# Kernel tuning notes

Measured on AMD Instinct MI355X. Metric: run time of the kernel, lower is better.

The kernel has to match this reference:

```python
import jax, jax.numpy as jnp
import numpy as np

VEC_DIM = 3          # Cl(3,0): 3 positive-signature basis vectors
BASIS_DIM = 1 << VEC_DIM  # 8 basis blades
BATCH, IN_F, OUT_F = 512, 512, 512


def cayley_table(n: int = VEC_DIM) -> np.ndarray:
    """Geometric-product tensor G[i, j, k] for Cl(n,0) with blades as bitmasks.
    e_a * e_b = sign(a,b) * e_{a XOR b}; Euclidean metric so e_i^2 = +1.
    Only 2^(2n) of the 2^(3n) entries are nonzero (highly sparse)."""
    dim = 1 << n
    G = np.zeros((dim, dim, dim), dtype=np.float32)
    for a in range(dim):
        for b in range(dim):
            # sign from counting transpositions to bring blade product to canonical order
            swaps, t = 0, a >> 1
            while t:
                swaps += bin(t & b).count("1")
                t >>= 1
            G[a, b, a ^ b] = -1.0 if (swaps & 1) else 1.0
    return G


def setup_inputs() -> dict:
    key = jax.random.key(0)
    kx, kw, kb = jax.random.split(key, 3)
    x = jax.random.normal(kx, (BATCH, IN_F, BASIS_DIM), dtype=jnp.float32)
    W = jax.random.normal(kw, (IN_F, OUT_F, BASIS_DIM), dtype=jnp.float32)
    b = jax.random.normal(kb, (OUT_F, BASIS_DIM), dtype=jnp.float32)
    G = jnp.asarray(cayley_table())  # exact Cl(3,0) geometric-product tensor
    return {"x": x, "W": W, "b": b, "G": G}


def reference(x, W, b, G):
    # out[b,o,k] = sum_{i,j,p} G[i,j,k] * x[b,p,i] * W[p,o,j]  (+ bias)
    out = jnp.einsum("ijk,bpi,poj->bok", G, x, W)
    return out + b
```

## Files before the change

kernel.cpp:

```cpp
#include <hip/hip_runtime.h>
#include <hip/hip_bf16.h>
#include <stdint.h>

typedef __attribute__((ext_vector_type(8))) short short8;
typedef __attribute__((ext_vector_type(4))) float floatx4;

__device__ __forceinline__ uint32_t pkbf(float a, float b) {
    unsigned short lo = __builtin_bit_cast(unsigned short, __float2bfloat16(a));
    unsigned short hi = __builtin_bit_cast(unsigned short, __float2bfloat16(b));
    return (uint32_t)lo | ((uint32_t)hi << 16);
}

__device__ __forceinline__ int gp_sign_neg(int a, int b) {
    int sw = 0, tt = a >> 1;
    while (tt) { sw += __popc(tt & b); tt >>= 1; }
    return sw & 1;
}

__global__ __launch_bounds__(256) void make_xT(const float* __restrict__ x,
                                               unsigned short* __restrict__ xT) {
    __shared__ unsigned short tile[8 * 512];
    const int b = blockIdx.x;
    const int t = threadIdx.x;
    const float4* xb = (const float4*)(x + (size_t)b * 4096);
    float4 f0 = xb[4 * t + 0], f1 = xb[4 * t + 1], f2 = xb[4 * t + 2], f3 = xb[4 * t + 3];
    float a0[8] = {f0.x, f0.y, f0.z, f0.w, f1.x, f1.y, f1.z, f1.w};
    float a1[8] = {f2.x, f2.y, f2.z, f2.w, f3.x, f3.y, f3.z, f3.w};
    uint32_t* tl = (uint32_t*)tile;
    #pragma unroll
    for (int i = 0; i < 8; ++i)
        tl[i * 256 + t] = pkbf(a0[i], a1[i]);
    __syncthreads();
    uint4* dst = (uint4*)(xT + (size_t)b * 4096);
    const uint4* src = (const uint4*)tile;
    dst[t] = src[t];
    dst[t + 256] = src[t + 256];
}

__global__ __launch_bounds__(256) void make_WT(const float* __restrict__ W,
                                               unsigned short* __restrict__ WT) {
    __shared__ unsigned short tile[8 * 64 * 24];
    const int t = threadIdx.x;
    const int o0 = blockIdx.x * 64, p0 = blockIdx.y * 16;
    const int o = t & 63, pq = t >> 6;
    float v[4][8];
    #pragma unroll
    for (int s = 0; s < 4; ++s) {
        const float4* src = (const float4*)(W + ((size_t)(p0 + pq * 4 + s) * 512 + o0 + o) * 8);
        float4 lo = src[0], hi = src[1];
        v[s][0] = lo.x; v[s][1] = lo.y; v[s][2] = lo.z; v[s][3] = lo.w;
        v[s][4] = hi.x; v[s][5] = hi.y; v[s][6] = hi.z; v[s][7] = hi.w;
    }
    #pragma unroll
    for (int j = 0; j < 8; ++j) {
        uint32_t* p = (uint32_t*)&tile[(j * 64 + o) * 24 + pq * 4];
        p[0] = pkbf(v[0][j], v[1][j]);
        p[1] = pkbf(v[2][j], v[3][j]);
    }
    __syncthreads();
    #pragma unroll
    for (int si = 0; si < 4; ++si) {
        int c = si * 256 + t;
        int j = c >> 7, oo = (c >> 1) & 63, h = c & 1;
        uint4 val = *(const uint4*)&tile[(j * 64 + oo) * 24 + h * 8];
        *(uint4*)&WT[((size_t)j * 512 + o0 + oo) * 512 + p0 + h * 8] = val;
    }
}

#define GLL(src, dstoff) \
    __builtin_amdgcn_global_load_lds((const __attribute__((address_space(1))) uint32_t*)(src), \
        (__attribute__((address_space(3))) uint32_t*)(smem + (dstoff)), 16, 0, 0)

__global__ __launch_bounds__(512, 2) void gp_gemm(
    const unsigned short* __restrict__ xT,
    const unsigned short* __restrict__ WT,
    const float* __restrict__ bias,
    float*       __restrict__ out)
{
    __shared__ __align__(16) unsigned char smem[81920];
    const int t = threadIdx.x;
    const int lane = t & 63;
    const int wave = t >> 6;
    const int wm = wave & 1;
    const int g  = wave >> 1;
    const int j0 = (g & 1) * 4;
    const int c0 = (g >> 1) * 2;
    const int l15 = lane & 15;
    const int q = lane >> 4;

    const int lin = blockIdx.y * 32 + blockIdx.x;
    const int cx = lin & 7, sx = lin >> 3;
    const int n_tile = (cx & 3) * 2 + (sx & 1);
    const int m_tile = (cx >> 2) * 16 + (sx >> 1);
    const int m0 = m_tile * 128;
    const int n0 = n_tile * 64;
    const int bg0 = m0 >> 3;

    const int sa_b = t >> 5, sa_i = (t >> 2) & 7, sa_cs = t & 3;
    const int sa_cl = sa_cs ^ ((sa_i & 3) ^ ((sa_i >> 2) & 1));
    const unsigned short* a_src = xT + ((size_t)(bg0 + sa_b) * 8 + sa_i) * 512 + sa_cl * 8;
    const unsigned short* b_srcs[4];
    #pragma unroll
    for (int si = 0; si < 4; ++si) {
        int s = si * 512 + t;
        int j = s >> 8, n = (s >> 2) & 63, cs = s & 3;
        int cl = cs ^ ((n >> 1) & 3);
        b_srcs[si] = WT + ((size_t)j * 512 + n0 + n) * 512 + cl * 8;
    }

    const int k_l = l15 & 7;
    const int j_l = j0 + q;
    const int i_l = k_l ^ j_l;
    const uint32_t xmask = gp_sign_neg(i_l, j_l) ? 0x80008000u : 0u;
    const int Sil = (i_l & 3) ^ ((i_l >> 2) & 1);
    const int a_off = (((wm * 8 + (l15 >> 3)) * 8 + i_l) * 4 + (c0 ^ Sil)) * 16;
    const int b_off = 8192 + ((j_l * 64 + l15) * 4 + (c0 ^ ((l15 >> 1) & 3))) * 16;

    floatx4 acc[4][4] = {};
    const int wbase = wave * 1024;

    GLL(a_src, wbase);
    #pragma unroll
    for (int si = 0; si < 4; ++si)
        GLL(b_srcs[si], 8192 + si * 8192 + wbase);

    for (int kt = 0; kt < 16; ++kt) {
        __syncthreads();
        const int cur = (kt & 1) * 40960;
        if (kt + 1 < 16) {
            const int nxt = ((kt + 1) & 1) * 40960;
            const int poff = (kt + 1) * 32;
            GLL(a_src + poff, nxt + wbase);
            #pragma unroll
            for (int si = 0; si < 4; ++si)
                GLL(b_srcs[si] + poff, nxt + 8192 + si * 8192 + wbase);
        }
        #pragma unroll
        for (int ss = 0; ss < 2; ++ss) {
            const int ax = ss * 16;
            short8 af[4], bf[4];
            #pragma unroll
            for (int tm = 0; tm < 4; ++tm) {
                af[tm] = *(const short8*)&smem[cur + ((a_off + tm * 1024) ^ ax)];
                uint32_t* u = (uint32_t*)&af[tm];
                u[0] ^= xmask; u[1] ^= xmask; u[2] ^= xmask; u[3] ^= xmask;
            }
            #pragma unroll
            for (int tn = 0; tn < 4; ++tn)
                bf[tn] = *(const short8*)&smem[cur + ((b_off + tn * 1024) ^ ax)];
            #pragma unroll
            for (int tm = 0; tm < 4; ++tm)
                #pragma unroll
                for (int tn = 0; tn < 4; ++tn)
                    acc[tm][tn] = __builtin_amdgcn_mfma_f32_16x16x32_bf16(
                        af[tm], bf[tn], acc[tm][tn], 0, 0, 0);
        }
    }

    __syncthreads();
    float* red = (float*)smem;
    if (g >= 2) {
        float* r = red + (wm * 2 + (g - 2)) * 4096;
        #pragma unroll
        for (int f = 0; f < 16; ++f)
            *(floatx4*)&r[f * 256 + lane * 4] = acc[f >> 2][f & 3];
    }
    __syncthreads();
    if (g < 2) {
        const float* r = red + (wm * 2 + g) * 4096;
        #pragma unroll
        for (int f = 0; f < 16; ++f)
            acc[f >> 2][f & 3] += *(const floatx4*)&r[f * 256 + lane * 4];
    }
    __syncthreads();
    if (g == 1) {
        float* r = red + wm * 4096;
        #pragma unroll
        for (int f = 0; f < 16; ++f)
            *(floatx4*)&r[f * 256 + lane * 4] = acc[f >> 2][f & 3];
    }
    __syncthreads();
    if (g == 0) {
        const float* r = red + wm * 4096;
        #pragma unroll
        for (int f = 0; f < 16; ++f)
            acc[f >> 2][f & 3] += *(const floatx4*)&r[f * 256 + lane * 4];
        #pragma unroll
        for (int tm = 0; tm < 4; ++tm)
            #pragma unroll
            for (int tn = 0; tn < 4; ++tn) {
                const int n = n0 + tn * 16 + l15;
                #pragma unroll
                for (int rr = 0; rr < 4; ++rr) {
                    const int m = m0 + wm * 64 + tm * 16 + q * 4 + rr;
                    const int bi = m >> 3, k = m & 7;
                    out[(size_t)bi * 4096 + n * 8 + k] = acc[tm][tn][rr] + bias[n * 8 + k];
                }
            }
    }
}

__device__ __align__(16) const uint32_t SGN[4][4] = {
    {0x00000000u, 0x80000000u, 0x80000000u, 0x80008000u},
    {0x80000000u, 0x00000000u, 0x00000000u, 0x00008000u},
    {0x80000000u, 0x80008000u, 0x00000000u, 0x80000000u},
    {0x00000000u, 0x00008000u, 0x80000000u, 0x00000000u},
};
__device__ __forceinline__ uint32_t swap16(uint32_t a) { return (a >> 16) | (a << 16); }
__device__ __forceinline__ uint4 xperm2(uint4 v, int kp) {
    const bool s1 = (kp & 1) != 0;
    uint32_t x1 = s1 ? v.y : v.x, y1 = s1 ? v.x : v.y, z1 = s1 ? v.w : v.z, w1 = s1 ? v.z : v.w;
    const bool s2 = (kp & 2) != 0;
    uint4 r; r.x = s2 ? z1 : x1; r.y = s2 ? w1 : y1; r.z = s2 ? x1 : z1; r.w = s2 ? y1 : w1;
    return r;
}
__global__ __launch_bounds__(512) void gp_linear_legacy(
    const float* __restrict__ xg_raw, const float* __restrict__ wg,
    const float* __restrict__ bias, float* __restrict__ out)
{
    __shared__ __align__(16) unsigned short As[128 * 64];
    __shared__ __align__(16) unsigned short Bs[8 * 64 * 8];
    const int t = threadIdx.x, lane = t & 63, wave = t >> 6;
    const int m0 = blockIdx.y * 128, n0 = blockIdx.x * 64;
    const int ap = t & 7, akp = (t >> 3) & 3, ab = t >> 5, ak0 = akp * 2;
    const uint4 mask = *(const uint4*)SGN[akp];
    const int wm = wave & 3, wn = wave >> 2, l15 = lane & 15, q = lane >> 4;
    floatx4 acc[2][2] = {};
    const float4* xg = (const float4*)xg_raw;
    const int bg0 = m0 >> 3;
    float4 ax0, ax1, bw0, bw1;
    {
        const size_t aidx = ((size_t)(bg0 + ab) * 512 + ap) * 2;
        ax0 = xg[aidx]; ax1 = xg[aidx + 1];
        const float* gsrc = wg + (((size_t)wave * 512 + n0) << 3) + (lane << 3);
        bw0 = *(const float4*)gsrc; bw1 = *(const float4*)(gsrc + 4);
    }
    for (int kt = 0; kt < 64; ++kt) {
        __syncthreads();
        {
            uint4 v;
            v.x = pkbf(ax0.x, ax0.y); v.y = pkbf(ax0.z, ax0.w);
            v.z = pkbf(ax1.x, ax1.y); v.w = pkbf(ax1.z, ax1.w);
            uint4 pk = xperm2(v, akp), r0, p1, r1;
            r0.x = pk.x ^ mask.x; r0.y = pk.y ^ mask.y; r0.z = pk.z ^ mask.z; r0.w = pk.w ^ mask.w;
            p1.x = swap16(pk.x); p1.y = swap16(pk.y); p1.z = swap16(pk.z); p1.w = swap16(pk.w);
            r1.x = p1.x ^ mask.x; r1.y = p1.y ^ mask.y; r1.z = p1.z ^ mask.z; r1.w = p1.w ^ mask.w;
            const int row0 = ab * 8 + ak0;
            *(uint4*)&As[row0 * 64 + ((ap ^ ak0) << 3)] = r0;
            *(uint4*)&As[(row0 + 1) * 64 + ((ap ^ (ak0 + 1)) << 3)] = r1;
        }
        {
            uint4 b0;
            b0.x = pkbf(bw0.x, bw0.y); b0.y = pkbf(bw0.z, bw0.w);
            b0.z = pkbf(bw1.x, bw1.y); b0.w = pkbf(bw1.z, bw1.w);
            *(uint4*)&Bs[t << 3] = b0;
        }
        __syncthreads();
        if (kt + 1 < 64) {
            const int p0n = (kt + 1) * 8;
            const size_t aidx = ((size_t)(bg0 + ab) * 512 + p0n + ap) * 2;
            ax0 = xg[aidx]; ax1 = xg[aidx + 1];
            const float* gsrc = wg + (((size_t)(p0n + wave) * 512 + n0) << 3) + (lane << 3);
            bw0 = *(const float4*)gsrc; bw1 = *(const float4*)(gsrc + 4);
        }
        #pragma unroll
        for (int ks = 0; ks < 2; ++ks) {
            const int cb = ks * 4 + q;
            short8 a[2], bfr[2];
            #pragma unroll
            for (int tm = 0; tm < 2; ++tm) {
                const int row = wm * 32 + tm * 16 + l15;
                a[tm] = *(const short8*)&As[row * 64 + ((cb ^ (l15 & 7)) << 3)];
            }
            #pragma unroll
            for (int tn = 0; tn < 2; ++tn) {
                const int nl = wn * 32 + tn * 16 + l15;
                bfr[tn] = *(const short8*)&Bs[((cb * 64) + nl) << 3];
            }
            #pragma unroll
            for (int tm = 0; tm < 2; ++tm)
                #pragma unroll
                for (int tn = 0; tn < 2; ++tn)
                    acc[tm][tn] = __builtin_amdgcn_mfma_f32_16x16x32_bf16(a[tm], bfr[tn], acc[tm][tn], 0, 0, 0);
        }
    }
    #pragma unroll
    for (int tm = 0; tm < 2; ++tm)
        #pragma unroll
        for (int tn = 0; tn < 2; ++tn) {
            const int n = n0 + wn * 32 + tn * 16 + l15;
            #pragma unroll
            for (int r = 0; r < 4; ++r) {
                const int m = m0 + wm * 32 + tm * 16 + q * 4 + r;
                const int bi = m >> 3, k = m & 7;
                out[(size_t)bi * 4096 + n * 8 + k] = acc[tm][tn][r] + bias[n * 8 + k];
            }
        }
}

extern "C" void kernel_launch(void* const* d_in, const int* in_sizes, int n_in,
                              void* d_out, int out_size, void* d_ws, size_t ws_size,
                              hipStream_t stream) {
    const float* x  = (const float*)d_in[0];
    const float* W  = (const float*)d_in[1];
    const float* bb = (const float*)d_in[2];
    float* out = (float*)d_out;

    if (ws_size >= 2u * 512u * 8u * 512u * sizeof(unsigned short)) {
        unsigned short* xT = (unsigned short*)d_ws;
        unsigned short* WT = xT + 512 * 8 * 512;
        make_xT<<<512, 256, 0, stream>>>(x, xT);
        make_WT<<<dim3(8, 32), 256, 0, stream>>>(W, WT);
        gp_gemm<<<dim3(32, 8), 512, 0, stream>>>(xT, WT, bb, out);
    } else {
        gp_linear_legacy<<<dim3(8, 32), dim3(512), 0, stream>>>(x, W, bb, out);
    }
}
```

Measured before the change: 95.21 us.

## Use Cl(3,0) matrix isomorphism to turn geometric product into 2x2 complex GEMM

Replaces the Cayley-table-driven GEMM, which folds 8 blade components into K and masks signs per lane, with the algebra isomorphism Cl(3,0) ≅ M2(C). x and W are packed into 2x2 complex matrix form (real/imag split into a real-valued block GEMM of size 1024x2048 by 2048x2048). The epilogue stages results in LDS and converts back to blade coefficients with bias added, writing out coalesced float4s. This cuts the multiply count relative to the dense 8x8 expansion and removes the per-fragment sign XORs, at the cost of extra add/sub work in the packing kernels, a larger workspace, and a more complex epilogue.

```diff
diff --git a/kernel.cpp b/kernel.cpp
--- a/kernel.cpp
+++ b/kernel.cpp
@@ -5,198 +5,217 @@
 typedef __attribute__((ext_vector_type(8))) short short8;
 typedef __attribute__((ext_vector_type(4))) float floatx4;
 
+__device__ __forceinline__ unsigned short bfu(float a) {
+    return __builtin_bit_cast(unsigned short, __float2bfloat16(a));
+}
 __device__ __forceinline__ uint32_t pkbf(float a, float b) {
-    unsigned short lo = __builtin_bit_cast(unsigned short, __float2bfloat16(a));
-    unsigned short hi = __builtin_bit_cast(unsigned short, __float2bfloat16(b));
-    return (uint32_t)lo | ((uint32_t)hi << 16);
-}
-
-__device__ __forceinline__ int gp_sign_neg(int a, int b) {
-    int sw = 0, tt = a >> 1;
-    while (tt) { sw += __popc(tt & b); tt >>= 1; }
-    return sw & 1;
-}
-
-__global__ __launch_bounds__(256) void make_xT(const float* __restrict__ x,
-                                               unsigned short* __restrict__ xT) {
-    __shared__ unsigned short tile[8 * 512];
+    return (uint32_t)bfu(a) | ((uint32_t)bfu(b) << 16);
+}
+
+
+__global__ __launch_bounds__(256) void pack_x(
+    const float* __restrict__ x, unsigned short* __restrict__ Abuf)
+{
+    __shared__ unsigned short TX[4][1024];
     const int b = blockIdx.x;
     const int t = threadIdx.x;
-    const float4* xb = (const float4*)(x + (size_t)b * 4096);
-    float4 f0 = xb[4 * t + 0], f1 = xb[4 * t + 1], f2 = xb[4 * t + 2], f3 = xb[4 * t + 3];
-    float a0[8] = {f0.x, f0.y, f0.z, f0.w, f1.x, f1.y, f1.z, f1.w};
-    float a1[8] = {f2.x, f2.y, f2.z, f2.w, f3.x, f3.y, f3.z, f3.w};
-    uint32_t* tl = (uint32_t*)tile;
-    #pragma unroll
-    for (int i = 0; i < 8; ++i)
-        tl[i * 256 + t] = pkbf(a0[i], a1[i]);
-    __syncthreads();
-    uint4* dst = (uint4*)(xT + (size_t)b * 4096);
-    const uint4* src = (const uint4*)tile;
-    dst[t] = src[t];
-    dst[t + 256] = src[t + 256];
-}
-
-__global__ __launch_bounds__(256) void make_WT(const float* __restrict__ W,
-                                               unsigned short* __restrict__ WT) {
-    __shared__ unsigned short tile[8 * 64 * 24];
+    const float4* src = (const float4*)(x + ((size_t)b * 512 + 2 * t) * 8);
+    float4 f[4] = {src[0], src[1], src[2], src[3]};
+    #pragma unroll
+    for (int pp = 0; pp < 2; ++pp) {
+        const float a0 = f[2*pp].x, a1 = f[2*pp].y, a2 = f[2*pp].z, a3 = f[2*pp].w;
+        const float a4 = f[2*pp+1].x, a5 = f[2*pp+1].y, a6 = f[2*pp+1].z, a7 = f[2*pp+1].w;
+        const int c = 4 * t + 2 * pp;
+        TX[0][c] = bfu(a0 + a4); TX[0][c+1] = bfu(a1 - a5);
+        TX[1][c] = bfu(a3 + a7); TX[1][c+1] = bfu(a6 - a2);
+        TX[2][c] = bfu(a1 + a5); TX[2][c+1] = bfu(a0 - a4);
+        TX[3][c] = bfu(a6 + a2); TX[3][c+1] = bfu(a7 - a3);
+    }
+    __syncthreads();
+    const int tr = t >> 6, off = (t & 63) * 16;
+    uint4* dst = (uint4*)(Abuf + (size_t)(2*b + (tr >> 1)) * 2048 + (tr & 1) * 1024 + off);
+    const uint4* s4 = (const uint4*)&TX[tr][off];
+    dst[0] = s4[0]; dst[1] = s4[1];
+}
+
+__global__ __launch_bounds__(256) void pack_w(
+    const float* __restrict__ W, unsigned short* __restrict__ BT)
+{
+    const int wb = blockIdx.x;
+    const int pbase = (wb & 7) * 64;
+    const int o0 = (wb >> 3) * 16;
     const int t = threadIdx.x;
-    const int o0 = blockIdx.x * 64, p0 = blockIdx.y * 16;
-    const int o = t & 63, pq = t >> 6;
-    float v[4][8];
-    #pragma unroll
-    for (int s = 0; s < 4; ++s) {
-        const float4* src = (const float4*)(W + ((size_t)(p0 + pq * 4 + s) * 512 + o0 + o) * 8);
+    const int pc = t & 15;
+    const int o = o0 + (t >> 4);
+    float R[4][2][2], I[4][2][2];
+    #pragma unroll
+    for (int u = 0; u < 4; ++u) {
+        const float4* src = (const float4*)(W + ((size_t)(pbase + pc * 4 + u) * 512 + o) * 8);
         float4 lo = src[0], hi = src[1];
-        v[s][0] = lo.x; v[s][1] = lo.y; v[s][2] = lo.z; v[s][3] = lo.w;
-        v[s][4] = hi.x; v[s][5] = hi.y; v[s][6] = hi.z; v[s][7] = hi.w;
-    }
-    #pragma unroll
-    for (int j = 0; j < 8; ++j) {
-        uint32_t* p = (uint32_t*)&tile[(j * 64 + o) * 24 + pq * 4];
-        p[0] = pkbf(v[0][j], v[1][j]);
-        p[1] = pkbf(v[2][j], v[3][j]);
-    }
-    __syncthreads();
-    #pragma unroll
-    for (int si = 0; si < 4; ++si) {
-        int c = si * 256 + t;
-        int j = c >> 7, oo = (c >> 1) & 63, h = c & 1;
-        uint4 val = *(const uint4*)&tile[(j * 64 + oo) * 24 + h * 8];
-        *(uint4*)&WT[((size_t)j * 512 + o0 + oo) * 512 + p0 + h * 8] = val;
-    }
+        R[u][0][0] = lo.x + hi.x;  I[u][0][0] = lo.w + hi.w;
+        R[u][0][1] = lo.y - hi.y;  I[u][0][1] = hi.z - lo.z;
+        R[u][1][0] = lo.y + hi.y;  I[u][1][0] = hi.z + lo.z;
+        R[u][1][1] = lo.x - hi.x;  I[u][1][1] = hi.w - lo.w;
+    }
+    const int kbase = 2 * pbase + pc * 8;
+    #pragma unroll
+    for (int part = 0; part < 2; ++part)
+        #pragma unroll
+        for (int pN = 0; pN < 2; ++pN)
+            #pragma unroll
+            for (int c = 0; c < 2; ++c) {
+                uint4 v; uint32_t* vv = (uint32_t*)&v;
+                #pragma unroll
+                for (int u = 0; u < 4; ++u) {
+                    const float v0 = (part == 0) ? (pN ? I[u][0][c] : R[u][0][c])
+                                                 : (pN ? R[u][0][c] : -I[u][0][c]);
+                    const float v1 = (part == 0) ? (pN ? I[u][1][c] : R[u][1][c])
+                                                 : (pN ? R[u][1][c] : -I[u][1][c]);
+                    vv[u] = pkbf(v0, v1);
+                }
+                const int n = 4 * o + 2 * pN + c;
+                *(uint4*)&BT[(size_t)n * 2048 + part * 1024 + kbase] = v;
+            }
 }
 
 #define GLL(src, dstoff) \
     __builtin_amdgcn_global_load_lds((const __attribute__((address_space(1))) uint32_t*)(src), \
         (__attribute__((address_space(3))) uint32_t*)(smem + (dstoff)), 16, 0, 0)
 
-__global__ __launch_bounds__(512, 2) void gp_gemm(
-    const unsigned short* __restrict__ xT,
-    const unsigned short* __restrict__ WT,
+__global__ __launch_bounds__(512, 2) void iso_gemm(
+    const unsigned short* __restrict__ AB,
+    const unsigned short* __restrict__ BB,
     const float* __restrict__ bias,
     float*       __restrict__ out)
 {
-    __shared__ __align__(16) unsigned char smem[81920];
-    const int t = threadIdx.x;
-    const int lane = t & 63;
-    const int wave = t >> 6;
-    const int wm = wave & 1;
+    __shared__ __align__(16) unsigned char smem[98304];
+    const int t = threadIdx.x, lane = t & 63, wave = t >> 6;
+    const int wn = wave & 1;
     const int g  = wave >> 1;
-    const int j0 = (g & 1) * 4;
-    const int c0 = (g >> 1) * 2;
-    const int l15 = lane & 15;
-    const int q = lane >> 4;
-
-    const int lin = blockIdx.y * 32 + blockIdx.x;
-    const int cx = lin & 7, sx = lin >> 3;
-    const int n_tile = (cx & 3) * 2 + (sx & 1);
-    const int m_tile = (cx >> 2) * 16 + (sx >> 1);
-    const int m0 = m_tile * 128;
-    const int n0 = n_tile * 64;
-    const int bg0 = m0 >> 3;
-
-    const int sa_b = t >> 5, sa_i = (t >> 2) & 7, sa_cs = t & 3;
-    const int sa_cl = sa_cs ^ ((sa_i & 3) ^ ((sa_i >> 2) & 1));
-    const unsigned short* a_src = xT + ((size_t)(bg0 + sa_b) * 8 + sa_i) * 512 + sa_cl * 8;
-    const unsigned short* b_srcs[4];
-    #pragma unroll
-    for (int si = 0; si < 4; ++si) {
-        int s = si * 512 + t;
-        int j = s >> 8, n = (s >> 2) & 63, cs = s & 3;
-        int cl = cs ^ ((n >> 1) & 3);
-        b_srcs[si] = WT + ((size_t)j * 512 + n0 + n) * 512 + cl * 8;
-    }
-
-    const int k_l = l15 & 7;
-    const int j_l = j0 + q;
-    const int i_l = k_l ^ j_l;
-    const uint32_t xmask = gp_sign_neg(i_l, j_l) ? 0x80008000u : 0u;
-    const int Sil = (i_l & 3) ^ ((i_l >> 2) & 1);
-    const int a_off = (((wm * 8 + (l15 >> 3)) * 8 + i_l) * 4 + (c0 ^ Sil)) * 16;
-    const int b_off = 8192 + ((j_l * 64 + l15) * 4 + (c0 ^ ((l15 >> 1) & 3))) * 16;
+    const int l15 = lane & 15, q = lane >> 4;
+
+    const int lin = blockIdx.y * 16 + blockIdx.x;
+    const int xcd = lin & 7, sx = lin >> 3;
+    const int tn = (xcd & 3) * 4 + (sx & 3);
+    const int tm = (xcd >> 2) * 8 + (sx >> 2);
+    const int m0 = tm * 64, v0 = tn * 128;
+
+    const unsigned short* a_srcs[2]; int a_dst[2];
+    #pragma unroll
+    for (int i = 0; i < 2; ++i) {
+        const int sl = (wave * 2 + i) * 64 + lane;
+        const int row = sl >> 4, slot = sl & 15, chunk = slot ^ (row & 7);
+        a_srcs[i] = AB + (size_t)(m0 + row) * 2048 + chunk * 8;
+        a_dst[i] = (wave * 2 + i) * 1024;
+    }
+    const unsigned short* b_srcs[4]; int b_dst[4];
+    #pragma unroll
+    for (int i = 0; i < 4; ++i) {
+        const int sl = (wave * 4 + i) * 64 + lane;
+        const int row = sl >> 4, slot = sl & 15, chunk = slot ^ (row & 7);
+        b_srcs[i] = BB + (size_t)(v0 + row) * 2048 + chunk * 8;
+        b_dst[i] = 16384 + (wave * 4 + i) * 1024;
+    }
+
+    const int chunk = g * 4 + q;
+    const int slot = chunk ^ (l15 & 7);
+    const int a_off = l15 * 256 + slot * 16;
+    const int b_off = 16384 + (wn * 64 + l15) * 256 + slot * 16;
 
     floatx4 acc[4][4] = {};
-    const int wbase = wave * 1024;
-
-    GLL(a_src, wbase);
-    #pragma unroll
-    for (int si = 0; si < 4; ++si)
-        GLL(b_srcs[si], 8192 + si * 8192 + wbase);
+
+    #pragma unroll
+    for (int i = 0; i < 2; ++i) GLL(a_srcs[i], a_dst[i]);
+    #pragma unroll
+    for (int i = 0; i < 4; ++i) GLL(b_srcs[i], b_dst[i]);
 
     for (int kt = 0; kt < 16; ++kt) {
         __syncthreads();
-        const int cur = (kt & 1) * 40960;
+        const int cur = (kt & 1) * 49152;
         if (kt + 1 < 16) {
-            const int nxt = ((kt + 1) & 1) * 40960;
-            const int poff = (kt + 1) * 32;
-            GLL(a_src + poff, nxt + wbase);
-            #pragma unroll
-            for (int si = 0; si < 4; ++si)
-                GLL(b_srcs[si] + poff, nxt + 8192 + si * 8192 + wbase);
-        }
-        #pragma unroll
-        for (int ss = 0; ss < 2; ++ss) {
-            const int ax = ss * 16;
-            short8 af[4], bf[4];
-            #pragma unroll
-            for (int tm = 0; tm < 4; ++tm) {
-                af[tm] = *(const short8*)&smem[cur + ((a_off + tm * 1024) ^ ax)];
-                uint32_t* u = (uint32_t*)&af[tm];
-                u[0] ^= xmask; u[1] ^= xmask; u[2] ^= xmask; u[3] ^= xmask;
-            }
-            #pragma unroll
-            for (int tn = 0; tn < 4; ++tn)
-                bf[tn] = *(const short8*)&smem[cur + ((b_off + tn * 1024) ^ ax)];
-            #pragma unroll
-            for (int tm = 0; tm < 4; ++tm)
-                #pragma unroll
-                for (int tn = 0; tn < 4; ++tn)
-                    acc[tm][tn] = __builtin_amdgcn_mfma_f32_16x16x32_bf16(
-                        af[tm], bf[tn], acc[tm][tn], 0, 0, 0);
-        }
+            const int nxt = ((kt + 1) & 1) * 49152;
+            const int poff = (kt + 1) * 128;
+            #pragma unroll
+            for (int i = 0; i < 2; ++i) GLL(a_srcs[i] + poff, nxt + a_dst[i]);
+            #pragma unroll
+            for (int i = 0; i < 4; ++i) GLL(b_srcs[i] + poff, nxt + b_dst[i]);
+        }
+        short8 af[4], bf[4];
+        #pragma unroll
+        for (int fm = 0; fm < 4; ++fm)
+            af[fm] = *(const short8*)&smem[cur + a_off + fm * 4096];
+        #pragma unroll
+        for (int fn = 0; fn < 4; ++fn)
+            bf[fn] = *(const short8*)&smem[cur + b_off + fn * 4096];
+        #pragma unroll
+        for (int fm = 0; fm < 4; ++fm)
+            #pragma unroll
+            for (int fn = 0; fn < 4; ++fn)
+                acc[fm][fn] = __builtin_amdgcn_mfma_f32_16x16x32_bf16(
+                    af[fm], bf[fn], acc[fm][fn], 0, 0, 0);
     }
 
     __syncthreads();
     float* red = (float*)smem;
     if (g >= 2) {
-        float* r = red + (wm * 2 + (g - 2)) * 4096;
+        float* r = red + (wn * 2 + (g - 2)) * 4096;
         #pragma unroll
         for (int f = 0; f < 16; ++f)
             *(floatx4*)&r[f * 256 + lane * 4] = acc[f >> 2][f & 3];
     }
     __syncthreads();
     if (g < 2) {
-        const float* r = red + (wm * 2 + g) * 4096;
+        const float* r = red + (wn * 2 + g) * 4096;
         #pragma unroll
         for (int f = 0; f < 16; ++f)
             acc[f >> 2][f & 3] += *(const floatx4*)&r[f * 256 + lane * 4];
     }
     __syncthreads();
     if (g == 1) {
-        float* r = red + wm * 4096;
+        float* r = red + wn * 4096;
         #pragma unroll
         for (int f = 0; f < 16; ++f)
             *(floatx4*)&r[f * 256 + lane * 4] = acc[f >> 2][f & 3];
     }
     __syncthreads();
+    float* Cf = (float*)(smem + 32768);
     if (g == 0) {
-        const float* r = red + wm * 4096;
+        const float* r = red + wn * 4096;
         #pragma unroll
         for (int f = 0; f < 16; ++f)
             acc[f >> 2][f & 3] += *(const floatx4*)&r[f * 256 + lane * 4];
         #pragma unroll
-        for (int tm = 0; tm < 4; ++tm)
-            #pragma unroll
-            for (int tn = 0; tn < 4; ++tn) {
-                const int n = n0 + tn * 16 + l15;
+        for (int fm = 0; fm < 4; ++fm)
+            #pragma unroll
+            for (int fn = 0; fn < 4; ++fn)
                 #pragma unroll
                 for (int rr = 0; rr < 4; ++rr) {
-                    const int m = m0 + wm * 64 + tm * 16 + q * 4 + rr;
-                    const int bi = m >> 3, k = m & 7;
-                    out[(size_t)bi * 4096 + n * 8 + k] = acc[tm][tn][rr] + bias[n * 8 + k];
+                    const int row = fm * 16 + q * 4 + rr;
+                    const int col = wn * 64 + fn * 16 + l15;
+                    Cf[row * 130 + col] = acc[fm][fn][rr];
                 }
-            }
+    }
+    __syncthreads();
+    const int b0 = m0 >> 1, o0 = v0 >> 2;
+    #pragma unroll
+    for (int rnd = 0; rnd < 2; ++rnd) {
+        const int pi = rnd * 512 + t;
+        const int o_l = pi & 31, b_l = pi >> 5;
+        const float* r0 = &Cf[(2 * b_l) * 130 + 4 * o_l];
+        const float* r1 = r0 + 130;
+        const float Cr00 = r0[0], Cr01 = r0[1], Ci00 = r0[2], Ci01 = r0[3];
+        const float Cr10 = r1[0], Cr11 = r1[1], Ci10 = r1[2], Ci11 = r1[3];
+        const float a0 = 0.5f * (Cr00 + Cr11), a7 = 0.5f * (Ci00 + Ci11);
+        const float a4 = 0.5f * (Cr00 - Cr11), a3 = 0.5f * (Ci00 - Ci11);
+        const float a1 = 0.5f * (Cr01 + Cr10), a6 = 0.5f * (Ci01 + Ci10);
+        const float a2 = 0.5f * (Ci10 - Ci01), a5 = 0.5f * (Cr10 - Cr01);
+        const int o = o0 + o_l, b = b0 + b_l;
+        const float* bp = bias + o * 8;
+        float4 lo = {a0 + bp[0], a1 + bp[1], a2 + bp[2], a3 + bp[3]};
+        float4 hi = {a4 + bp[4], a5 + bp[5], a6 + bp[6], a7 + bp[7]};
+        float* op = out + ((size_t)b * 512 + o) * 8;
+        *(float4*)op = lo;
+        *(float4*)(op + 4) = hi;
     }
 }
 
@@ -224,7 +243,7 @@
     const int m0 = blockIdx.y * 128, n0 = blockIdx.x * 64;
     const int ap = t & 7, akp = (t >> 3) & 3, ab = t >> 5, ak0 = akp * 2;
     const uint4 mask = *(const uint4*)SGN[akp];
-    const int wm = wave & 3, wn = wave >> 2, l15 = lane & 15, q = lane >> 4;
+    const int wm = wave & 3, wnn = wave >> 2, l15 = lane & 15, q = lane >> 4;
     floatx4 acc[2][2] = {};
     const float4* xg = (const float4*)xg_raw;
     const int bg0 = m0 >> 3;
@@ -268,32 +287,32 @@
             const int cb = ks * 4 + q;
             short8 a[2], bfr[2];
             #pragma unroll
-            for (int tm = 0; tm < 2; ++tm) {
-                const int row = wm * 32 + tm * 16 + l15;
-                a[tm] = *(const short8*)&As[row * 64 + ((cb ^ (l15 & 7)) << 3)];
+            for (int fm = 0; fm < 2; ++fm) {
+                const int row = wm * 32 + fm * 16 + l15;
+                a[fm] = *(const short8*)&As[row * 64 + ((cb ^ (l15 & 7)) << 3)];
             }
             #pragma unroll
-            for (int tn = 0; tn < 2; ++tn) {
-                const int nl = wn * 32 + tn * 16 + l15;
-                bfr[tn] = *(const short8*)&Bs[((cb * 64) + nl) << 3];
+            for (int fn = 0; fn < 2; ++fn) {
+                const int nl = wnn * 32 + fn * 16 + l15;
+                bfr[fn] = *(const short8*)&Bs[((cb * 64) + nl) << 3];
             }
             #pragma unroll
-            for (int tm = 0; tm < 2; ++tm)
+            for (int fm = 0; fm < 2; ++fm)
                 #pragma unroll
-                for (int tn = 0; tn < 2; ++tn)
-                    acc[tm][tn] = __builtin_amdgcn_mfma_f32_16x16x32_bf16(a[tm], bfr[tn], acc[tm][tn], 0, 0, 0);
-        }
-    }
-    #pragma unroll
-    for (int tm = 0; tm < 2; ++tm)
-        #pragma unroll
-        for (int tn = 0; tn < 2; ++tn) {
-            const int n = n0 + wn * 32 + tn * 16 + l15;
+                for (int fn = 0; fn < 2; ++fn)
+                    acc[fm][fn] = __builtin_amdgcn_mfma_f32_16x16x32_bf16(a[fm], bfr[fn], acc[fm][fn], 0, 0, 0);
+        }
+    }
+    #pragma unroll
+    for (int fm = 0; fm < 2; ++fm)
+        #pragma unroll
+        for (int fn = 0; fn < 2; ++fn) {
+            const int n = n0 + wnn * 32 + fn * 16 + l15;
             #pragma unroll
             for (int r = 0; r < 4; ++r) {
-                const int m = m0 + wm * 32 + tm * 16 + q * 4 + r;
+                const int m = m0 + wm * 32 + fm * 16 + q * 4 + r;
                 const int bi = m >> 3, k = m & 7;
-                out[(size_t)bi * 4096 + n * 8 + k] = acc[tm][tn][r] + bias[n * 8 + k];
+                out[(size_t)bi * 4096 + n * 8 + k] = acc[fm][fn][r] + bias[n * 8 + k];
             }
         }
 }
@@ -306,12 +325,14 @@
     const float* bb = (const float*)d_in[2];
     float* out = (float*)d_out;
 
-    if (ws_size >= 2u * 512u * 8u * 512u * sizeof(unsigned short)) {
-        unsigned short* xT = (unsigned short*)d_ws;
-        unsigned short* WT = xT + 512 * 8 * 512;
-        make_xT<<<512, 256, 0, stream>>>(x, xT);
-        make_WT<<<dim3(8, 32), 256, 0, stream>>>(W, WT);
-        gp_gemm<<<dim3(32, 8), 512, 0, stream>>>(xT, WT, bb, out);
+    const size_t abytes = (size_t)1024 * 2048 * sizeof(unsigned short);
+    const size_t bbytes = (size_t)2048 * 2048 * sizeof(unsigned short);
+    if (ws_size >= abytes + bbytes) {
+        unsigned short* Abuf = (unsigned short*)d_ws;
+        unsigned short* Bbuf = (unsigned short*)((char*)d_ws + abytes);
+        pack_x<<<512, 256, 0, stream>>>(x, Abuf);
+        pack_w<<<256, 256, 0, stream>>>(W, Bbuf);
+        iso_gemm<<<dim3(16, 16), 512, 0, stream>>>(Abuf, Bbuf, bb, out);
     } else {
         gp_linear_legacy<<<dim3(8, 32), dim3(512), 0, stream>>>(x, W, bb, out);
     }
```

Result: no change. 94.05 us (-1.2%).
